# Kernel tuning notes

Measured on AMD Instinct MI355X. Metric: run time of the kernel, lower is better.

Reference implementation:

```python
import jax, jax.numpy as jnp
import numpy as np


def setup_inputs() -> dict:
    key = jax.random.key(0)
    k_x, k_qkv, k_proj, k_bias = jax.random.split(key, 4)
    b, n, dim = 4, 8192, 512
    h, w = 8, 256
    x = jax.random.normal(k_x, (b, n, dim), dtype=jnp.float32)
    # Linear weights stored as [in, out] (transpose of torch's [out, in])
    Wqkv = jax.random.normal(k_qkv, (dim, 3 * dim), dtype=jnp.float32) * 0.02
    bqkv = jnp.zeros((3 * dim,), dtype=jnp.float32)
    Wproj = jax.random.normal(k_proj, (dim, dim), dtype=jnp.float32) * 0.02
    bproj = jnp.zeros((dim,), dtype=jnp.float32)
    # torch init is zeros; use small randn so the bias path is exercised
    attn_bias = jax.random.normal(k_bias, (h, w, w), dtype=jnp.float32) * 0.02
    return {"x": x, "Wqkv": Wqkv, "bqkv": bqkv, "Wproj": Wproj,
            "bproj": bproj, "attn_bias": attn_bias}


def reference(x, Wqkv, bqkv, Wproj, bproj, attn_bias):
    b, n, c = x.shape
    h, w, _ = attn_bias.shape
    d = c // h
    nw = n // w  # number of non-overlapping windows (n divisible by w)
    qkv = (x @ Wqkv + bqkv).reshape(b, n, 3, h, d)
    q, k, v = jnp.moveaxis(qkv, 2, 0)  # each [b, n, h, d]

    def to_windows(t):
        # [b, n, h, d] -> [b, h, nw, w, d]
        return t.reshape(b, nw, w, h, d).transpose(0, 3, 1, 2, 4)

    q, k, v = to_windows(q), to_windows(k), to_windows(v)
    scale = d ** -0.5
    # block-local attention: [b, h, nw, w, w]
    attn = jnp.einsum('bhnqd,bhnkd->bhnqk', q, k) * scale + attn_bias[None, :, None]
    attn = jax.nn.softmax(attn, axis=-1)
    out = jnp.einsum('bhnqk,bhnkd->bhnqd', attn, v)
    # [b, h, nw, w, d] -> [b, n, h*d]
    out = out.transpose(0, 2, 3, 1, 4).reshape(b, n, c)
    return out @ Wproj + bproj
```

## Files before the change

kernel.cpp:

```cpp
#include <hip/hip_runtime.h>

typedef unsigned short u16;
typedef unsigned int u32;
typedef __bf16 bf16x8 __attribute__((ext_vector_type(8)));
typedef float f32x4 __attribute__((ext_vector_type(4)));


__device__ __forceinline__ u16 f2bf(float f) {
  u32 u = __builtin_bit_cast(u32, f);
  u32 r = (u + 0x7fffu + ((u >> 16) & 1u)) >> 16;
  return (u16)r;
}
__device__ __forceinline__ u32 pk2(float a, float b) {
  return (u32)f2bf(a) | ((u32)f2bf(b) << 16);
}
__device__ __forceinline__ f32x4 mfma16(bf16x8 a, bf16x8 b, f32x4 c) {
  return __builtin_amdgcn_mfma_f32_16x16x32_bf16(a, b, c, 0, 0, 0);
}
__device__ __forceinline__ void glds16(const void* g, void* l) {
  typedef __attribute__((address_space(1))) void as1_void;
  typedef __attribute__((address_space(3))) void as3_void;
  __builtin_amdgcn_global_load_lds((as1_void*)g, (as3_void*)l, 16, 0, 0);
}


__device__ __forceinline__ void transpose_body(const float* __restrict__ in,
                                               u16* __restrict__ out,
                                               int N, int n0, int k0) {
  __shared__ float t[32][33];
  int tx = threadIdx.x & 31, ty = threadIdx.x >> 5;
#pragma unroll
  for (int s = 0; s < 32; s += 8)
    t[ty + s][tx] = in[(long)(k0 + ty + s) * N + n0 + tx];
  __syncthreads();
#pragma unroll
  for (int s = 0; s < 32; s += 8)
    out[(long)(n0 + ty + s) * 512 + k0 + tx] = f2bf(t[tx][ty + s]);
}

__launch_bounds__(256)
__global__ void prep_k(const float* __restrict__ x, u16* __restrict__ xbf,
                       const float* __restrict__ Wqkv, u16* __restrict__ wqkvT,
                       const float* __restrict__ Wproj, u16* __restrict__ wprojT,
                       const float* __restrict__ bias, float* __restrict__ biasT) {
  const int id = blockIdx.x;
  if (id < 8192) {
    long i = ((long)id * 256 + threadIdx.x) * 8;
    float4 f0 = *(const float4*)(x + i);
    float4 f1 = *(const float4*)(x + i + 4);
    uint4 o;
    o.x = pk2(f0.x, f0.y);
    o.y = pk2(f0.z, f0.w);
    o.z = pk2(f1.x, f1.y);
    o.w = pk2(f1.z, f1.w);
    *(uint4*)(xbf + i) = o;
  } else if (id < 8960) {
    int bx = id - 8192;
    transpose_body(Wqkv, wqkvT, 1536, (bx % 48) * 32, (bx / 48) * 32);
  } else if (id < 9216) {
    int bx = id - 8960;
    transpose_body(Wproj, wprojT, 512, (bx & 15) * 32, (bx >> 4) * 32);
  } else {
    int hb = id - 9216;
    int h = hb >> 4, rt = hb & 15;
    int lane = threadIdx.x & 63;
    int quad = lane >> 4, l15 = lane & 15;
    int jtg = threadIdx.x >> 6;
    const float L = 1.44269504f;
#pragma unroll
    for (int i = 0; i < 4; ++i) {
      int jt = jtg * 4 + i;
      float4 v = *(const float4*)&bias[((long)h * 256 + rt * 16 + l15) * 256 + jt * 16 + quad * 4];
      v.x *= L; v.y *= L; v.z *= L; v.w *= L;
      *(float4*)&biasT[(((long)hb * 16 + jt) * 64 + lane) * 4] = v;
    }
  }
}


template <int EPI>
__device__ __forceinline__ void gemm_body(const u16* __restrict__ A, const u16* __restrict__ Bt,
                                          const float* __restrict__ bias,
                                          u16* __restrict__ oqk, u16* __restrict__ ovt,
                                          float* __restrict__ ofp,
                                          long arow0, long brow0) {
  constexpr int K = 512;
  __shared__ u16 Asm[8192];
  __shared__ u16 Bsm[8192];

  const int tid = threadIdx.x;
  const int wave = tid >> 6, lane = tid & 63;
  const int quad = lane >> 4, l15 = lane & 15;
  const int wm = wave >> 1, wn = wave & 1;
  const int gsw = quad ^ ((l15 >> 1) & 3);

  f32x4 acc[4][4] = {};

  for (int k0 = 0; k0 < K; k0 += 64) {
#pragma unroll
    for (int rd = 0; rd < 4; ++rd) {
      int flat = rd * 256 + tid;
      int c = flat >> 9, row = (flat >> 2) & 127, gp = flat & 3;
      int g = gp ^ ((row >> 1) & 3);
      const long koff = k0 + c * 32 + g * 8;
      glds16(A + (arow0 + row) * K + koff, &Asm[(rd * 256 + wave * 64) * 8]);
      glds16(Bt + (brow0 + row) * K + koff, &Bsm[(rd * 256 + wave * 64) * 8]);
    }
    __syncthreads();
#pragma unroll
    for (int c = 0; c < 2; ++c) {
      bf16x8 af[4], bfr[4];
#pragma unroll
      for (int i = 0; i < 4; ++i)
        af[i] = *(const bf16x8*)&Asm[c * 4096 + (wm * 64 + i * 16 + l15) * 32 + gsw * 8];
#pragma unroll
      for (int j = 0; j < 4; ++j)
        bfr[j] = *(const bf16x8*)&Bsm[c * 4096 + (wn * 64 + j * 16 + l15) * 32 + gsw * 8];
#pragma unroll
      for (int i = 0; i < 4; ++i)
#pragma unroll
        for (int j = 0; j < 4; ++j)
          acc[i][j] = mfma16(af[i], bfr[j], acc[i][j]);
    }
    __syncthreads();
  }

#pragma unroll
  for (int j = 0; j < 4; ++j) {
    const int C = (int)brow0 + wn * 64 + j * 16 + l15;
    const float bc = bias[C];
#pragma unroll
    for (int i = 0; i < 4; ++i) {
      const long R0 = arow0 + wm * 64 + i * 16 + quad * 4;
      float v4[4];
#pragma unroll
      for (int r = 0; r < 4; ++r) v4[r] = acc[i][j][r] + bc;
      if constexpr (EPI == 0) {
        if (C < 1024) {
#pragma unroll
          for (int r = 0; r < 4; ++r) oqk[(R0 + r) * 1024 + C] = f2bf(v4[r]);
        } else {
          const int hc = (C >> 6) & 7, dc = C & 63;
          const int b = (int)(R0 >> 13), n0 = (int)(R0 & 8191);
          uint2 w;
          w.x = pk2(v4[0], v4[1]);
          w.y = pk2(v4[2], v4[3]);
          *(uint2*)&ovt[((long)(b * 8 + hc) * 64 + dc) * 8192 + n0] = w;
        }
      } else {
#pragma unroll
        for (int r = 0; r < 4; ++r) ofp[(R0 + r) * 512 + C] = v4[r];
      }
    }
  }
}


__launch_bounds__(256)
__global__ void qkv_gemm_k(const u16* __restrict__ A, const u16* __restrict__ Bt,
                           const float* __restrict__ bias,
                           u16* __restrict__ oqk, u16* __restrict__ ovt) {
  int bid = blockIdx.x;
  int xcd = bid & 7, i = bid >> 3;
  int nt = i % 12, mtl = i / 12;
  gemm_body<0>(A, Bt, bias, oqk, ovt, nullptr,
               (long)(xcd * 32 + mtl) * 128, (long)nt * 128);
}

__launch_bounds__(256)
__global__ void proj_gemm_k(const u16* __restrict__ A, const u16* __restrict__ Bt,
                            const float* __restrict__ bias, float* __restrict__ ofp) {
  int bid = blockIdx.x;
  int xcd = bid & 7, i = bid >> 3;
  int nt = i & 3, mtl = i >> 2;
  gemm_body<1>(A, Bt, bias, nullptr, nullptr, ofp,
               (long)(xcd * 32 + mtl) * 128, (long)nt * 128);
}


__launch_bounds__(512, 4)
__global__ void attn_win(const u16* __restrict__ qk, const u16* __restrict__ vtb,
                         const float* __restrict__ biasT, u16* __restrict__ og) {
  __shared__ __align__(16) u16 kS[16384];
  __shared__ __align__(16) u16 vS[16384];
  __shared__ __align__(16) u16 pS[8][1024];

  const int tid = threadIdx.x;
  const int wave = tid >> 6, lane = tid & 63;
  const int quad = lane >> 4, l15 = lane & 15;
  const int gsw = quad ^ ((l15 >> 1) & 3);

  const int wi = blockIdx.x;
  const int xcd = wi & 7, hi = (wi >> 3) & 7, wl = wi >> 6;
  const int win = xcd * 16 + wl;
  const int nwi = win & 31, bi = win >> 5;
  const long grow = (long)bi * 8192 + nwi * 256;
  const u16* qp = qk + grow * 1024 + hi * 64;
  const u16* kp = qp + 512;
  const u16* vp = vtb + (long)(bi * 8 + hi) * 64 * 8192 + nwi * 256;

  bf16x8 bq[2][2];
#pragma unroll
  for (int sc = 0; sc < 2; ++sc) {
    const int q0 = wave * 32 + sc * 16;
    bq[sc][0] = *(const bf16x8*)&qp[(long)(q0 + l15) * 1024 + quad * 8];
    bq[sc][1] = *(const bf16x8*)&qp[(long)(q0 + l15) * 1024 + 32 + quad * 8];
  }

#pragma unroll
  for (int it = 0; it < 4; ++it) {
    int flat = it * 512 + tid;
    int t = flat >> 3, dg = flat & 7;
    int c = dg >> 2, gp = (dg & 3) ^ ((t >> 1) & 3);
    int4 val = *(const int4*)&kp[(long)t * 1024 + dg * 8];
    *(int4*)&kS[c * 8192 + t * 32 + gp * 8] = val;
  }
#pragma unroll
  for (int it = 0; it < 4; ++it) {
    int flat = it * 512 + tid;
    int d = flat >> 5, tg = flat & 31;
    int kk = tg >> 2, gp = (tg & 3) ^ ((d >> 1) & 3);
    int4 val = *(const int4*)&vp[(long)d * 8192 + tg * 8];
    *(int4*)&vS[kk * 2048 + d * 32 + gp * 8] = val;
  }
  __syncthreads();

  u16* Pw = pS[wave];
  const float cscale = 0.18033688f;

#pragma unroll
  for (int sc = 0; sc < 2; ++sc) {
    const int q0 = wave * 32 + sc * 16;
    const int rt = wave * 2 + sc;
    const float* bT = &biasT[(long)(hi * 16 + rt) * 16 * 64 * 4];

    f32x4 sum4 = {0.f, 0.f, 0.f, 0.f};
    f32x4 o[4] = {};

#pragma unroll
    for (int m = 0; m < 4; ++m) {
#pragma unroll
      for (int j2 = 0; j2 < 4; ++j2) {
        const int jt = m * 4 + j2;
        bf16x8 a0 = *(const bf16x8*)&kS[(jt * 16 + l15) * 32 + gsw * 8];
        bf16x8 a1 = *(const bf16x8*)&kS[8192 + (jt * 16 + l15) * 32 + gsw * 8];
        f32x4 z = {0.f, 0.f, 0.f, 0.f};
        __builtin_amdgcn_s_setprio(1);
        z = mfma16(a0, bq[sc][0], z);
        z = mfma16(a1, bq[sc][1], z);
        __builtin_amdgcn_s_setprio(0);
        f32x4 bb = *(const f32x4*)&bT[(long)jt * 256 + lane * 4];
        f32x4 p;
#pragma unroll
        for (int r = 0; r < 4; ++r) {
          p[r] = __builtin_exp2f(z[r] * cscale + bb[r]);
          sum4[r] += p[r];
        }
        const int gp = ((jt & 1) * 2 + (quad >> 1)) ^ ((l15 >> 1) & 3);
        const int slot = (jt >> 1) & 1;
        uint2 w;
        w.x = pk2(p[0], p[1]);
        w.y = pk2(p[2], p[3]);
        *(uint2*)&Pw[slot * 512 + l15 * 32 + gp * 8 + (quad & 1) * 4] = w;
      }
#pragma unroll
      for (int kk2 = 0; kk2 < 2; ++kk2) {
        const int kk = m * 2 + kk2;
        bf16x8 bp = *(const bf16x8*)&Pw[kk2 * 512 + l15 * 32 + gsw * 8];
        __builtin_amdgcn_s_setprio(1);
#pragma unroll
        for (int dt = 0; dt < 4; ++dt) {
          bf16x8 av = *(const bf16x8*)&vS[kk * 2048 + (dt * 16 + l15) * 32 + gsw * 8];
          o[dt] = mfma16(av, bp, o[dt]);
        }
        __builtin_amdgcn_s_setprio(0);
      }
    }

    float sum = (sum4[0] + sum4[1]) + (sum4[2] + sum4[3]);
    sum += __shfl_xor(sum, 16);
    sum += __shfl_xor(sum, 32);
    const float inv = 1.0f / sum;

    const long rowoff = (grow + q0 + l15) * 512 + hi * 64 + quad * 4;
#pragma unroll
    for (int dt = 0; dt < 4; ++dt) {
      uint2 w;
      w.x = pk2(o[dt][0] * inv, o[dt][1] * inv);
      w.y = pk2(o[dt][2] * inv, o[dt][3] * inv);
      *(uint2*)&og[rowoff + dt * 16] = w;
    }
  }
}


extern "C" void kernel_launch(void* const* d_in, const int* in_sizes, int n_in,
                              void* d_out, int out_size, void* d_ws, size_t ws_size,
                              hipStream_t stream) {
  const float* x     = (const float*)d_in[0];
  const float* Wqkv  = (const float*)d_in[1];
  const float* bqkv  = (const float*)d_in[2];
  const float* Wproj = (const float*)d_in[3];
  const float* bproj = (const float*)d_in[4];
  const float* abias = (const float*)d_in[5];
  float* out = (float*)d_out;

  char* ws = (char*)d_ws;
  u16*   qkp    = (u16*)(ws);
  u16*   vtb    = (u16*)(ws + 67108864L);
  u16*   wqkvT  = (u16*)(ws + 100663296L);
  u16*   wprojT = (u16*)(ws + 102236160L);
  float* biasTp = (float*)(ws + 102760448L);
  u16*   xbf    = (u16*)(ws + 104857600L);
  u16*   attnout = xbf;

  prep_k<<<9344, 256, 0, stream>>>(x, xbf, Wqkv, wqkvT, Wproj, wprojT, abias, biasTp);
  qkv_gemm_k<<<3072, 256, 0, stream>>>(xbf, wqkvT, bqkv, qkp, vtb);
  attn_win<<<1024, 512, 0, stream>>>(qkp, vtb, biasTp, attnout);
  proj_gemm_k<<<1024, 256, 0, stream>>>(attnout, wprojT, bproj, out);
}
```

Measured before the change: 271.7 us.

## Feed softmax probabilities to PV MFMA directly from registers using 16x16x16 bf16

Drops the per-wave LDS staging buffer for the probability tile. The QK^T accumulator layout already matches the B-operand layout of the 16x16x16 bf16 MFMA, so each 16-key chunk of P is converted in registers and multiplied against V slices loaded with matching swizzled offsets. This removes the LDS writes and reads for P and shrinks shared memory use. The cost is twice as many smaller-K MFMAs for the PV product, which have lower throughput per instruction than the 16x16x32 form.

```diff
diff --git a/kernel.cpp b/kernel.cpp
--- a/kernel.cpp
+++ b/kernel.cpp
@@ -3,6 +3,7 @@
 typedef unsigned short u16;
 typedef unsigned int u32;
 typedef __bf16 bf16x8 __attribute__((ext_vector_type(8)));
+typedef short s16x4 __attribute__((ext_vector_type(4)));
 typedef float f32x4 __attribute__((ext_vector_type(4)));
 
 
@@ -16,6 +17,20 @@
 }
 __device__ __forceinline__ f32x4 mfma16(bf16x8 a, bf16x8 b, f32x4 c) {
   return __builtin_amdgcn_mfma_f32_16x16x32_bf16(a, b, c, 0, 0, 0);
+}
+__device__ __forceinline__ f32x4 mfma16k16(s16x4 a, s16x4 b, f32x4 c) {
+#if __has_builtin(__builtin_amdgcn_mfma_f32_16x16x16_bf16)
+  typedef __bf16 bf16x4_t __attribute__((ext_vector_type(4)));
+  return __builtin_amdgcn_mfma_f32_16x16x16_bf16(
+      __builtin_bit_cast(bf16x4_t, a), __builtin_bit_cast(bf16x4_t, b), c, 0, 0, 0);
+#elif __has_builtin(__builtin_amdgcn_mfma_f32_16x16x16bf16_1k)
+  return __builtin_amdgcn_mfma_f32_16x16x16bf16_1k(a, b, c, 0, 0, 0);
+#else
+  f32x4 d;
+  asm volatile("v_mfma_f32_16x16x16_bf16 %0, %1, %2, %3"
+               : "=v"(d) : "v"(a), "v"(b), "v"(c));
+  return d;
+#endif
 }
 __device__ __forceinline__ void glds16(const void* g, void* l) {
   typedef __attribute__((address_space(1))) void as1_void;
@@ -183,12 +198,13 @@
                          const float* __restrict__ biasT, u16* __restrict__ og) {
   __shared__ __align__(16) u16 kS[16384];
   __shared__ __align__(16) u16 vS[16384];
-  __shared__ __align__(16) u16 pS[8][1024];
 
   const int tid = threadIdx.x;
   const int wave = tid >> 6, lane = tid & 63;
   const int quad = lane >> 4, l15 = lane & 15;
-  const int gsw = quad ^ ((l15 >> 1) & 3);
+  const int sw = (l15 >> 1) & 3;
+  const int gsw = quad ^ sw;
+  const int qh = quad >> 1, q1 = quad & 1;
 
   const int wi = blockIdx.x;
   const int xcd = wi & 7, hi = (wi >> 3) & 7, wl = wi >> 6;
@@ -225,7 +241,6 @@
   }
   __syncthreads();
 
-  u16* Pw = pS[wave];
   const float cscale = 0.18033688f;
 
 #pragma unroll
@@ -238,43 +253,36 @@
     f32x4 o[4] = {};
 
 #pragma unroll
-    for (int m = 0; m < 4; ++m) {
-#pragma unroll
-      for (int j2 = 0; j2 < 4; ++j2) {
-        const int jt = m * 4 + j2;
-        bf16x8 a0 = *(const bf16x8*)&kS[(jt * 16 + l15) * 32 + gsw * 8];
-        bf16x8 a1 = *(const bf16x8*)&kS[8192 + (jt * 16 + l15) * 32 + gsw * 8];
-        f32x4 z = {0.f, 0.f, 0.f, 0.f};
-        __builtin_amdgcn_s_setprio(1);
-        z = mfma16(a0, bq[sc][0], z);
-        z = mfma16(a1, bq[sc][1], z);
-        __builtin_amdgcn_s_setprio(0);
-        f32x4 bb = *(const f32x4*)&bT[(long)jt * 256 + lane * 4];
-        f32x4 p;
-#pragma unroll
-        for (int r = 0; r < 4; ++r) {
-          p[r] = __builtin_exp2f(z[r] * cscale + bb[r]);
-          sum4[r] += p[r];
-        }
-        const int gp = ((jt & 1) * 2 + (quad >> 1)) ^ ((l15 >> 1) & 3);
-        const int slot = (jt >> 1) & 1;
-        uint2 w;
-        w.x = pk2(p[0], p[1]);
-        w.y = pk2(p[2], p[3]);
-        *(uint2*)&Pw[slot * 512 + l15 * 32 + gp * 8 + (quad & 1) * 4] = w;
+    for (int jt = 0; jt < 16; ++jt) {
+      bf16x8 a0 = *(const bf16x8*)&kS[(jt * 16 + l15) * 32 + gsw * 8];
+      bf16x8 a1 = *(const bf16x8*)&kS[8192 + (jt * 16 + l15) * 32 + gsw * 8];
+      f32x4 z = {0.f, 0.f, 0.f, 0.f};
+      __builtin_amdgcn_s_setprio(1);
+      z = mfma16(a0, bq[sc][0], z);
+      z = mfma16(a1, bq[sc][1], z);
+      __builtin_amdgcn_s_setprio(0);
+      f32x4 bb = *(const f32x4*)&bT[(long)jt * 256 + lane * 4];
+      f32x4 p;
+#pragma unroll
+      for (int r = 0; r < 4; ++r) {
+        p[r] = __builtin_exp2f(z[r] * cscale + bb[r]);
+        sum4[r] += p[r];
       }
-#pragma unroll
-      for (int kk2 = 0; kk2 < 2; ++kk2) {
-        const int kk = m * 2 + kk2;
-        bf16x8 bp = *(const bf16x8*)&Pw[kk2 * 512 + l15 * 32 + gsw * 8];
-        __builtin_amdgcn_s_setprio(1);
-#pragma unroll
-        for (int dt = 0; dt < 4; ++dt) {
-          bf16x8 av = *(const bf16x8*)&vS[kk * 2048 + (dt * 16 + l15) * 32 + gsw * 8];
-          o[dt] = mfma16(av, bp, o[dt]);
-        }
-        __builtin_amdgcn_s_setprio(0);
+      s16x4 bp;
+      bp[0] = (short)f2bf(p[0]);
+      bp[1] = (short)f2bf(p[1]);
+      bp[2] = (short)f2bf(p[2]);
+      bp[3] = (short)f2bf(p[3]);
+      const int kk = jt >> 1;
+      const int gp = (((jt & 1) << 1) | qh) ^ sw;
+      const int vbase = kk * 2048 + l15 * 32 + gp * 8 + q1 * 4;
+      __builtin_amdgcn_s_setprio(1);
+#pragma unroll
+      for (int dt = 0; dt < 4; ++dt) {
+        s16x4 av = *(const s16x4*)&vS[vbase + dt * 512];
+        o[dt] = mfma16k16(av, bp, o[dt]);
       }
+      __builtin_amdgcn_s_setprio(0);
     }
 
     float sum = (sum4[0] + sum4[1]) + (sum4[2] + sum4[3]);
```

Measured after the change: 284.7 us. 1.05x slower.
